# Kernel optimization log

Measured on AMD Instinct MI355X. Metric: run time of the kernel, lower is better.

Reference implementation:

```python
import jax, jax.numpy as jnp
import numpy as np

B, S, D, C = 8, 2048, 1024, 4096

def setup_inputs() -> dict:
    key = jax.random.key(0)
    k1, k2 = jax.random.split(key)
    x = jax.random.normal(k1, (B, S, D), dtype=jnp.float32)
    label_repr = jax.random.normal(k2, (C, D), dtype=jnp.float32)
    return {"x": x, "label_repr": label_repr}

def reference(x, label_repr):
    # A = softmax(x @ label_repr^T) over label axis: [B,S,C]
    scores = jnp.einsum('bsd,cd->bsc', x, label_repr)
    A = jax.nn.softmax(scores, axis=-1)
    # output = A^T @ x : [B,C,D]
    output = jnp.einsum('bsc,bsd->bcd', A, x)
    return (output, A)
```

## Files before the change

### kernel.cpp

```cpp
#include <hip/hip_runtime.h>
#include <hip/hip_bf16.h>

#define NB 8
#define NS 2048
#define ND 1024
#define NC 4096
#define NM (NB*NS)

typedef __attribute__((ext_vector_type(8))) short bf16x8;
typedef __attribute__((ext_vector_type(4))) float floatx4;
typedef unsigned short ushort_t;

__device__ __forceinline__ unsigned short f2bf(float f) {
  unsigned int u = __builtin_bit_cast(unsigned int, f);
  u += 0x7fffu + ((u >> 16) & 1u);
  return (unsigned short)(u >> 16);
}
__device__ __forceinline__ float bf2f(unsigned short h) {
  unsigned int u = ((unsigned int)h) << 16;
  return __builtin_bit_cast(float, u);
}

__device__ __forceinline__ void load_lds16(const void* g, void* s) {
  __builtin_amdgcn_global_load_lds(
      (const __attribute__((address_space(1))) char*)g,
      (__attribute__((address_space(3))) char*)s, 16, 0, 0);
}


__global__ __launch_bounds__(256)
void prep_L(const float* __restrict__ L, ushort_t* __restrict__ Lh,
            ushort_t* __restrict__ Ll) {
  const size_t i = ((size_t)blockIdx.x * 256 + threadIdx.x) * 4;
  float4 v = *(const float4*)(L + i);
  ushort4 h, lo;
  h.x = f2bf(v.x); lo.x = f2bf(v.x - bf2f(h.x));
  h.y = f2bf(v.y); lo.y = f2bf(v.y - bf2f(h.y));
  h.z = f2bf(v.z); lo.z = f2bf(v.z - bf2f(h.z));
  h.w = f2bf(v.w); lo.w = f2bf(v.w - bf2f(h.w));
  *(ushort4*)(Lh + i) = h;
  *(ushort4*)(Ll + i) = lo;
}

__global__ __launch_bounds__(256)
void prep_x(const float* __restrict__ x, ushort_t* __restrict__ xh,
            ushort_t* __restrict__ xl, ushort_t* __restrict__ xT) {
  __shared__ unsigned int tile[256 * 17];
  const int b = blockIdx.z;
  const int s0 = blockIdx.y << 5;
  const int d0 = blockIdx.x << 8;
  const int tid = threadIdx.x;
  const int sp = tid & 15, cg = tid >> 4;
  const int r0 = 2 * sp, r1 = r0 + 1;
  const float* xb = x + (size_t)b * NS * ND;
  ushort_t* xhb = xh + (size_t)b * NS * ND;
  ushort_t* xlb = xl + (size_t)b * NS * ND;
  #pragma unroll
  for (int i = 0; i < 4; ++i) {
    const int crel = cg * 4 + i * 64;
    const int col = d0 + crel;
    float4 v0 = *(const float4*)(xb + (size_t)(s0 + r0) * ND + col);
    float4 v1 = *(const float4*)(xb + (size_t)(s0 + r1) * ND + col);
    ushort4 h0, l0, h1, l1;
    h0.x = f2bf(v0.x); l0.x = f2bf(v0.x - bf2f(h0.x));
    h0.y = f2bf(v0.y); l0.y = f2bf(v0.y - bf2f(h0.y));
    h0.z = f2bf(v0.z); l0.z = f2bf(v0.z - bf2f(h0.z));
    h0.w = f2bf(v0.w); l0.w = f2bf(v0.w - bf2f(h0.w));
    h1.x = f2bf(v1.x); l1.x = f2bf(v1.x - bf2f(h1.x));
    h1.y = f2bf(v1.y); l1.y = f2bf(v1.y - bf2f(h1.y));
    h1.z = f2bf(v1.z); l1.z = f2bf(v1.z - bf2f(h1.z));
    h1.w = f2bf(v1.w); l1.w = f2bf(v1.w - bf2f(h1.w));
    *(ushort4*)(xhb + (size_t)(s0 + r0) * ND + col) = h0;
    *(ushort4*)(xlb + (size_t)(s0 + r0) * ND + col) = l0;
    *(ushort4*)(xhb + (size_t)(s0 + r1) * ND + col) = h1;
    *(ushort4*)(xlb + (size_t)(s0 + r1) * ND + col) = l1;
    tile[(crel + 0) * 17 + sp] = (unsigned)h0.x | ((unsigned)h1.x << 16);
    tile[(crel + 1) * 17 + sp] = (unsigned)h0.y | ((unsigned)h1.y << 16);
    tile[(crel + 2) * 17 + sp] = (unsigned)h0.z | ((unsigned)h1.z << 16);
    tile[(crel + 3) * 17 + sp] = (unsigned)h0.w | ((unsigned)h1.w << 16);
  }
  __syncthreads();
  unsigned tmp[16];
  #pragma unroll
  for (int k = 0; k < 16; ++k) tmp[k] = tile[tid * 17 + k];
  ushort_t* dst = xT + ((size_t)b * ND + d0 + tid) * NS + s0;
  #pragma unroll
  for (int k = 0; k < 4; ++k) *(uint4*)(dst + k * 8) = *(uint4*)&tmp[k * 4];
}

__global__ __launch_bounds__(256, 2)
void gemm1_v2(const ushort_t* __restrict__ xh, const ushort_t* __restrict__ xl,
              const ushort_t* __restrict__ Lh, const ushort_t* __restrict__ Ll,
              float* __restrict__ sc) {
  __shared__ ushort_t sAh[128 * 32];
  __shared__ ushort_t sAl[128 * 32];
  __shared__ ushort_t sBh[128 * 32];
  __shared__ ushort_t sBl[128 * 32];
  const int tid = threadIdx.x;
  const int m0 = blockIdx.y << 7;
  const int n0 = blockIdx.x << 7;
  const int w = tid >> 6, l = tid & 63;
  const int wm = (w >> 1) << 6;
  const int wn = (w & 1) << 6;
  const int lrow = l & 15, quad = l >> 4;
  const int srow = l >> 2;
  const int skol = (l & 3) << 3;

  floatx4 acc[4][4] = {};

  for (int k0 = 0; k0 < ND; k0 += 32) {
    __syncthreads();
    #pragma unroll
    for (int q = 0; q < 2; ++q) {
      const int row = w * 32 + q * 16 + srow;
      const size_t ga = (size_t)(m0 + row) * ND + k0 + skol;
      const size_t gb = (size_t)(n0 + row) * ND + k0 + skol;
      const int lo = w * 1024 + q * 512;
      load_lds16(xh + ga, &sAh[lo]);
      load_lds16(xl + ga, &sAl[lo]);
      load_lds16(Lh + gb, &sBh[lo]);
      load_lds16(Ll + gb, &sBl[lo]);
    }
    __syncthreads();
    bf16x8 ah[4], bh[4], t[4];
    #pragma unroll
    for (int i = 0; i < 4; ++i) ah[i] = *(const bf16x8*)&sAh[(wm + i*16 + lrow)*32 + quad*8];
    #pragma unroll
    for (int j = 0; j < 4; ++j) bh[j] = *(const bf16x8*)&sBh[(wn + j*16 + lrow)*32 + quad*8];
    #pragma unroll
    for (int i = 0; i < 4; ++i)
      #pragma unroll
      for (int j = 0; j < 4; ++j)
        acc[i][j] = __builtin_amdgcn_mfma_f32_16x16x32_bf16(ah[i], bh[j], acc[i][j], 0, 0, 0);
    #pragma unroll
    for (int i = 0; i < 4; ++i) t[i] = *(const bf16x8*)&sAl[(wm + i*16 + lrow)*32 + quad*8];
    #pragma unroll
    for (int i = 0; i < 4; ++i)
      #pragma unroll
      for (int j = 0; j < 4; ++j)
        acc[i][j] = __builtin_amdgcn_mfma_f32_16x16x32_bf16(t[i], bh[j], acc[i][j], 0, 0, 0);
    #pragma unroll
    for (int j = 0; j < 4; ++j) t[j] = *(const bf16x8*)&sBl[(wn + j*16 + lrow)*32 + quad*8];
    #pragma unroll
    for (int i = 0; i < 4; ++i)
      #pragma unroll
      for (int j = 0; j < 4; ++j)
        acc[i][j] = __builtin_amdgcn_mfma_f32_16x16x32_bf16(ah[i], t[j], acc[i][j], 0, 0, 0);
  }

  float* op = sc + (size_t)(m0 + wm + quad * 4) * NC + (n0 + wn + lrow);
  #pragma unroll
  for (int i = 0; i < 4; ++i)
    #pragma unroll
    for (int r = 0; r < 4; ++r)
      #pragma unroll
      for (int j = 0; j < 4; ++j)
        op[(size_t)(i * 16 + r) * NC + j * 16] = acc[i][j][r];
}

__global__ __launch_bounds__(256)
void softmax_T(float* __restrict__ A, ushort_t* __restrict__ AT) {
  __shared__ float sm[32], sli[32];
  __shared__ unsigned int tile[256 * 17];
  const int s0 = blockIdx.x << 5;
  const int b = s0 >> 11;
  const int sl0 = s0 & (NS - 1);
  const int tid = threadIdx.x;
  const int w = tid >> 6, l = tid & 63;

  float m[8], su[8];
  #pragma unroll
  for (int r = 0; r < 8; ++r) { m[r] = -3.0e38f; su[r] = 0.f; }
  for (int ch = 0; ch < 16; ++ch) {
    #pragma unroll
    for (int r = 0; r < 8; ++r) {
      float4 v = *(const float4*)(A + (size_t)(s0 + w * 8 + r) * NC + ch * 256 + (l << 2));
      float mx = fmaxf(fmaxf(v.x, v.y), fmaxf(v.z, v.w));
      float nm = fmaxf(m[r], mx);
      su[r] = su[r] * __expf(m[r] - nm) +
              __expf(v.x - nm) + __expf(v.y - nm) + __expf(v.z - nm) + __expf(v.w - nm);
      m[r] = nm;
    }
  }
  #pragma unroll
  for (int r = 0; r < 8; ++r) {
    #pragma unroll
    for (int off = 32; off; off >>= 1) {
      float om = __shfl_xor(m[r], off);
      float os = __shfl_xor(su[r], off);
      float nm = fmaxf(m[r], om);
      su[r] = su[r] * __expf(m[r] - nm) + os * __expf(om - nm);
      m[r] = nm;
    }
    if (l == 0) { sm[w * 8 + r] = m[r]; sli[w * 8 + r] = 1.0f / su[r]; }
  }
  __syncthreads();

  const int sp = tid & 15, cg = tid >> 4;
  const int r0 = 2 * sp, r1 = r0 + 1;
  const float M0 = sm[r0], I0 = sli[r0];
  const float M1 = sm[r1], I1 = sli[r1];
  float* A0 = A + (size_t)(s0 + r0) * NC;
  float* A1 = A + (size_t)(s0 + r1) * NC;
  for (int ch = 0; ch < 16; ++ch) {
    const int cb = ch << 8;
    #pragma unroll
    for (int i = 0; i < 4; ++i) {
      const int crel = cg * 4 + i * 64;
      float4 v0 = *(const float4*)(A0 + cb + crel);
      float4 v1 = *(const float4*)(A1 + cb + crel);
      float4 p0, p1;
      p0.x = __expf(v0.x - M0) * I0; p0.y = __expf(v0.y - M0) * I0;
      p0.z = __expf(v0.z - M0) * I0; p0.w = __expf(v0.w - M0) * I0;
      p1.x = __expf(v1.x - M1) * I1; p1.y = __expf(v1.y - M1) * I1;
      p1.z = __expf(v1.z - M1) * I1; p1.w = __expf(v1.w - M1) * I1;
      *(float4*)(A0 + cb + crel) = p0;
      *(float4*)(A1 + cb + crel) = p1;
      tile[(crel + 0) * 17 + sp] = (unsigned)f2bf(p0.x) | ((unsigned)f2bf(p1.x) << 16);
      tile[(crel + 1) * 17 + sp] = (unsigned)f2bf(p0.y) | ((unsigned)f2bf(p1.y) << 16);
      tile[(crel + 2) * 17 + sp] = (unsigned)f2bf(p0.z) | ((unsigned)f2bf(p1.z) << 16);
      tile[(crel + 3) * 17 + sp] = (unsigned)f2bf(p0.w) | ((unsigned)f2bf(p1.w) << 16);
    }
    __syncthreads();
    unsigned tmp[16];
    #pragma unroll
    for (int k = 0; k < 16; ++k) tmp[k] = tile[tid * 17 + k];
    ushort_t* dst = AT + ((size_t)b * NC + cb + tid) * NS + sl0;
    #pragma unroll
    for (int k = 0; k < 4; ++k) *(uint4*)(dst + k * 8) = *(uint4*)&tmp[k * 4];
    __syncthreads();
  }
}

__global__ __launch_bounds__(256, 2)
void gemm2_v2(const ushort_t* __restrict__ AT, const ushort_t* __restrict__ xT,
              float* __restrict__ out) {
  __shared__ ushort_t sA[128 * 32];
  __shared__ ushort_t sX[128 * 32];
  const int tid = threadIdx.x;
  const int b = blockIdx.z;
  const ushort_t* Ab = AT + (size_t)b * NC * NS;
  const ushort_t* xb = xT + (size_t)b * ND * NS;
  float* ob = out + (size_t)b * NC * ND;
  const int m0 = blockIdx.y << 7;
  const int n0 = blockIdx.x << 7;
  const int w = tid >> 6, l = tid & 63;
  const int wm = (w >> 1) << 6;
  const int wn = (w & 1) << 6;
  const int lrow = l & 15, quad = l >> 4;
  const int srow = l >> 2;
  const int skol = (l & 3) << 3;

  floatx4 acc[4][4] = {};

  for (int k0 = 0; k0 < NS; k0 += 32) {
    __syncthreads();
    #pragma unroll
    for (int q = 0; q < 2; ++q) {
      const int row = w * 32 + q * 16 + srow;
      const int lo = w * 1024 + q * 512;
      load_lds16(Ab + (size_t)(m0 + row) * NS + k0 + skol, &sA[lo]);
      load_lds16(xb + (size_t)(n0 + row) * NS + k0 + skol, &sX[lo]);
    }
    __syncthreads();
    bf16x8 af[4], bg[4];
    #pragma unroll
    for (int i = 0; i < 4; ++i) af[i] = *(const bf16x8*)&sA[(wm + i*16 + lrow)*32 + quad*8];
    #pragma unroll
    for (int j = 0; j < 4; ++j) bg[j] = *(const bf16x8*)&sX[(wn + j*16 + lrow)*32 + quad*8];
    #pragma unroll
    for (int i = 0; i < 4; ++i)
      #pragma unroll
      for (int j = 0; j < 4; ++j)
        acc[i][j] = __builtin_amdgcn_mfma_f32_16x16x32_bf16(af[i], bg[j], acc[i][j], 0, 0, 0);
  }

  float* op = ob + (size_t)(m0 + wm + quad * 4) * ND + (n0 + wn + lrow);
  #pragma unroll
  for (int i = 0; i < 4; ++i)
    #pragma unroll
    for (int r = 0; r < 4; ++r)
      #pragma unroll
      for (int j = 0; j < 4; ++j)
        op[(size_t)(i * 16 + r) * ND + j * 16] = acc[i][j][r];
}


__global__ __launch_bounds__(256, 2)
void gemm1_scores(const float* __restrict__ x, const float* __restrict__ L,
                  float* __restrict__ sc) {
  __shared__ unsigned short sAh[128*40];
  __shared__ unsigned short sAl[128*40];
  __shared__ unsigned short sBh[128*40];
  __shared__ unsigned short sBl[128*40];
  const int tid = threadIdx.x;
  const int m0 = blockIdx.y << 7;
  const int n0 = blockIdx.x << 7;
  const int w  = tid >> 6;
  const int l  = tid & 63;
  const int wm = (w >> 1) << 6;
  const int wn = (w & 1) << 6;
  const int lrow = l & 15;
  const int quad = l >> 4;
  floatx4 acc[4][4] = {};
  const int srow = tid >> 3;
  const int scol = (tid & 7) << 2;
  const float* xa = x + (size_t)(m0 + srow) * ND + scol;
  const float* lb = L + (size_t)(n0 + srow) * ND + scol;
  for (int k0 = 0; k0 < ND; k0 += 32) {
    float4 av[4], bv[4];
    #pragma unroll
    for (int p = 0; p < 4; ++p) {
      av[p] = *(const float4*)(xa + (size_t)(p*32) * ND + k0);
      bv[p] = *(const float4*)(lb + (size_t)(p*32) * ND + k0);
    }
    __syncthreads();
    #pragma unroll
    for (int p = 0; p < 4; ++p) {
      const int r = srow + p*32;
      ushort4 h, lo;
      h.x = f2bf(av[p].x); lo.x = f2bf(av[p].x - bf2f(h.x));
      h.y = f2bf(av[p].y); lo.y = f2bf(av[p].y - bf2f(h.y));
      h.z = f2bf(av[p].z); lo.z = f2bf(av[p].z - bf2f(h.z));
      h.w = f2bf(av[p].w); lo.w = f2bf(av[p].w - bf2f(h.w));
      *(ushort4*)&sAh[r*40 + scol] = h;
      *(ushort4*)&sAl[r*40 + scol] = lo;
      h.x = f2bf(bv[p].x); lo.x = f2bf(bv[p].x - bf2f(h.x));
      h.y = f2bf(bv[p].y); lo.y = f2bf(bv[p].y - bf2f(h.y));
      h.z = f2bf(bv[p].z); lo.z = f2bf(bv[p].z - bf2f(h.z));
      h.w = f2bf(bv[p].w); lo.w = f2bf(bv[p].w - bf2f(h.w));
      *(ushort4*)&sBh[r*40 + scol] = h;
      *(ushort4*)&sBl[r*40 + scol] = lo;
    }
    __syncthreads();
    bf16x8 ah[4], bh[4], t[4];
    #pragma unroll
    for (int i = 0; i < 4; ++i) ah[i] = *(const bf16x8*)&sAh[(wm + i*16 + lrow)*40 + quad*8];
    #pragma unroll
    for (int j = 0; j < 4; ++j) bh[j] = *(const bf16x8*)&sBh[(wn + j*16 + lrow)*40 + quad*8];
    #pragma unroll
    for (int i = 0; i < 4; ++i)
      #pragma unroll
      for (int j = 0; j < 4; ++j)
        acc[i][j] = __builtin_amdgcn_mfma_f32_16x16x32_bf16(ah[i], bh[j], acc[i][j], 0, 0, 0);
    #pragma unroll
    for (int i = 0; i < 4; ++i) t[i] = *(const bf16x8*)&sAl[(wm + i*16 + lrow)*40 + quad*8];
    #pragma unroll
    for (int i = 0; i < 4; ++i)
      #pragma unroll
      for (int j = 0; j < 4; ++j)
        acc[i][j] = __builtin_amdgcn_mfma_f32_16x16x32_bf16(t[i], bh[j], acc[i][j], 0, 0, 0);
    #pragma unroll
    for (int j = 0; j < 4; ++j) t[j] = *(const bf16x8*)&sBl[(wn + j*16 + lrow)*40 + quad*8];
    #pragma unroll
    for (int i = 0; i < 4; ++i)
      #pragma unroll
      for (int j = 0; j < 4; ++j)
        acc[i][j] = __builtin_amdgcn_mfma_f32_16x16x32_bf16(ah[i], t[j], acc[i][j], 0, 0, 0);
  }
  float* op = sc + (size_t)(m0 + wm + quad*4) * NC + (n0 + wn + lrow);
  #pragma unroll
  for (int i = 0; i < 4; ++i)
    #pragma unroll
    for (int r = 0; r < 4; ++r)
      #pragma unroll
      for (int j = 0; j < 4; ++j)
        op[(size_t)(i*16 + r) * NC + j*16] = acc[i][j][r];
}

__global__ __launch_bounds__(256)
void softmax_rows(float* __restrict__ A) {
  float* row = A + (size_t)blockIdx.x * NC;
  const int tid = threadIdx.x;
  float4 v[4];
  float mx = -3.0e38f;
  #pragma unroll
  for (int i = 0; i < 4; ++i) {
    v[i] = *(const float4*)(row + (tid << 2) + (i << 10));
    mx = fmaxf(mx, fmaxf(fmaxf(v[i].x, v[i].y), fmaxf(v[i].z, v[i].w)));
  }
  #pragma unroll
  for (int off = 32; off > 0; off >>= 1) mx = fmaxf(mx, __shfl_xor(mx, off));
  __shared__ float red[4];
  if ((tid & 63) == 0) red[tid >> 6] = mx;
  __syncthreads();
  mx = fmaxf(fmaxf(red[0], red[1]), fmaxf(red[2], red[3]));
  float s = 0.f;
  #pragma unroll
  for (int i = 0; i < 4; ++i) {
    v[i].x = __expf(v[i].x - mx); v[i].y = __expf(v[i].y - mx);
    v[i].z = __expf(v[i].z - mx); v[i].w = __expf(v[i].w - mx);
    s += (v[i].x + v[i].y) + (v[i].z + v[i].w);
  }
  #pragma unroll
  for (int off = 32; off > 0; off >>= 1) s += __shfl_xor(s, off);
  __syncthreads();
  if ((tid & 63) == 0) red[tid >> 6] = s;
  __syncthreads();
  s = (red[0] + red[1]) + (red[2] + red[3]);
  const float inv = 1.0f / s;
  #pragma unroll
  for (int i = 0; i < 4; ++i) {
    v[i].x *= inv; v[i].y *= inv; v[i].z *= inv; v[i].w *= inv;
    *(float4*)(row + (tid << 2) + (i << 10)) = v[i];
  }
}

__global__ __launch_bounds__(256, 2)
void gemm2_out(const float* __restrict__ A, const float* __restrict__ x,
               float* __restrict__ out) {
  __shared__ unsigned short sA[128*40];
  __shared__ unsigned short sX[128*40];
  const int tid = threadIdx.x;
  const float* Ab = A + (size_t)blockIdx.z * NS * NC;
  const float* xb = x + (size_t)blockIdx.z * NS * ND;
  float* ob = out + (size_t)blockIdx.z * NC * ND;
  const int m0 = blockIdx.y << 7;
  const int n0 = blockIdx.x << 7;
  const int w  = tid >> 6;
  const int l  = tid & 63;
  const int wm = (w >> 1) << 6;
  const int wn = (w & 1) << 6;
  const int lrow = l & 15;
  const int quad = l >> 4;
  floatx4 acc[4][4] = {};
  const int sp0 = tid & 15;
  const int cg0 = tid >> 4;
  for (int k0 = 0; k0 < NS; k0 += 32) {
    float4 a[2][2], xv[2][2];
    const int s = k0 + sp0*2;
    #pragma unroll
    for (int p = 0; p < 2; ++p) {
      const int c4 = (cg0 + p*16) << 2;
      a[p][0]  = *(const float4*)(Ab + (size_t)s     * NC + m0 + c4);
      a[p][1]  = *(const float4*)(Ab + (size_t)(s+1) * NC + m0 + c4);
      xv[p][0] = *(const float4*)(xb + (size_t)s     * ND + n0 + c4);
      xv[p][1] = *(const float4*)(xb + (size_t)(s+1) * ND + n0 + c4);
    }
    __syncthreads();
    #pragma unroll
    for (int p = 0; p < 2; ++p) {
      const int c4 = (cg0 + p*16) << 2;
      const float* fa0 = (const float*)&a[p][0];
      const float* fa1 = (const float*)&a[p][1];
      const float* fx0 = (const float*)&xv[p][0];
      const float* fx1 = (const float*)&xv[p][1];
      #pragma unroll
      for (int i = 0; i < 4; ++i) {
        const unsigned int pa = (unsigned int)f2bf(fa0[i]) | ((unsigned int)f2bf(fa1[i]) << 16);
        const unsigned int px = (unsigned int)f2bf(fx0[i]) | ((unsigned int)f2bf(fx1[i]) << 16);
        *(unsigned int*)&sA[(c4 + i)*40 + sp0*2] = pa;
        *(unsigned int*)&sX[(c4 + i)*40 + sp0*2] = px;
      }
    }
    __syncthreads();
    bf16x8 af[4], bg[4];
    #pragma unroll
    for (int i = 0; i < 4; ++i) af[i] = *(const bf16x8*)&sA[(wm + i*16 + lrow)*40 + quad*8];
    #pragma unroll
    for (int j = 0; j < 4; ++j) bg[j] = *(const bf16x8*)&sX[(wn + j*16 + lrow)*40 + quad*8];
    #pragma unroll
    for (int i = 0; i < 4; ++i)
      #pragma unroll
      for (int j = 0; j < 4; ++j)
        acc[i][j] = __builtin_amdgcn_mfma_f32_16x16x32_bf16(af[i], bg[j], acc[i][j], 0, 0, 0);
  }
  float* op = ob + (size_t)(m0 + wm + quad*4) * ND + (n0 + wn + lrow);
  #pragma unroll
  for (int i = 0; i < 4; ++i)
    #pragma unroll
    for (int r = 0; r < 4; ++r)
      #pragma unroll
      for (int j = 0; j < 4; ++j)
        op[(size_t)(i*16 + r) * ND + j*16] = acc[i][j][r];
}


extern "C" void kernel_launch(void* const* d_in, const int* in_sizes, int n_in,
                              void* d_out, int out_size, void* d_ws, size_t ws_size,
                              hipStream_t stream) {
  const float* x = (const float*)d_in[0];
  const float* L = (const float*)d_in[1];
  float* out = (float*)d_out;
  float* A   = out + (size_t)NB * NC * ND;

  const size_t EL_X  = (size_t)NB * NS * ND;
  const size_t EL_L  = (size_t)NC * ND;
  const size_t EL_AT = (size_t)NB * NC * NS;
  const size_t need  = (3 * EL_X + 2 * EL_L + EL_AT) * sizeof(ushort_t);

  if (ws_size >= need) {
    ushort_t* xh = (ushort_t*)d_ws;
    ushort_t* xl = xh + EL_X;
    ushort_t* xT = xl + EL_X;
    ushort_t* Lh = xT + EL_X;
    ushort_t* Ll = Lh + EL_L;
    ushort_t* AT = Ll + EL_L;
    prep_L<<<dim3((NC * ND) / 1024), 256, 0, stream>>>(L, Lh, Ll);
    prep_x<<<dim3(ND / 256, NS / 32, NB), 256, 0, stream>>>(x, xh, xl, xT);
    gemm1_v2<<<dim3(NC / 128, NM / 128), 256, 0, stream>>>(xh, xl, Lh, Ll, A);
    softmax_T<<<dim3(NM / 32), 256, 0, stream>>>(A, AT);
    gemm2_v2<<<dim3(ND / 128, NC / 128, NB), 256, 0, stream>>>(AT, xT, out);
  } else {
    gemm1_scores<<<dim3(NC / 128, NM / 128), 256, 0, stream>>>(x, L, A);
    softmax_rows<<<dim3(NM), 256, 0, stream>>>(A);
    gemm2_out<<<dim3(ND / 128, NC / 128, NB), 256, 0, stream>>>(A, x, out);
  }
}
```

Measured before the change: 1.166 ms.

## Fuse softmax row stats into GEMM1 epilogue and swizzle LDS tiles

GEMM1 now computes a per-tile row max and sum-of-exp in its epilogue and writes them to scratch space in the output buffer. The softmax kernel merges these partials, so it no longer does a full read pass over the scores. Both GEMMs also switch to a combined, XOR-swizzled LDS layout to avoid bank conflicts, and GEMM2 now uses a K step of 64. The costs are that the partials share the output buffer before GEMM2 overwrites it, and GEMM1 gains shuffles and an extra sync in its epilogue.

```diff
diff --git a/kernel.cpp b/kernel.cpp
--- a/kernel.cpp
+++ b/kernel.cpp
@@ -89,13 +89,12 @@
 }
 
 __global__ __launch_bounds__(256, 2)
-void gemm1_v2(const ushort_t* __restrict__ xh, const ushort_t* __restrict__ xl,
+void gemm1_v3(const ushort_t* __restrict__ xh, const ushort_t* __restrict__ xl,
               const ushort_t* __restrict__ Lh, const ushort_t* __restrict__ Ll,
-              float* __restrict__ sc) {
-  __shared__ ushort_t sAh[128 * 32];
-  __shared__ ushort_t sAl[128 * 32];
-  __shared__ ushort_t sBh[128 * 32];
-  __shared__ ushort_t sBl[128 * 32];
+              float* __restrict__ sc, float* __restrict__ pmax,
+              float* __restrict__ psum) {
+  __shared__ ushort_t sA[128 * 64];
+  __shared__ ushort_t sB[128 * 64];
   const int tid = threadIdx.x;
   const int m0 = blockIdx.y << 7;
   const int n0 = blockIdx.x << 7;
@@ -103,44 +102,45 @@
   const int wm = (w >> 1) << 6;
   const int wn = (w & 1) << 6;
   const int lrow = l & 15, quad = l >> 4;
-  const int srow = l >> 2;
-  const int skol = (l & 3) << 3;
+
+  const int rsub = l >> 3;
+  const int kg   = (l & 7) ^ rsub;
+  const int koff = (kg & 3) << 3;
+  const ushort_t* pax = (kg & 4) ? xl : xh;
+  const ushort_t* pbx = (kg & 4) ? Ll : Lh;
+
+  const int sw = (quad ^ (lrow & 7)) << 3;
 
   floatx4 acc[4][4] = {};
 
   for (int k0 = 0; k0 < ND; k0 += 32) {
     __syncthreads();
     #pragma unroll
-    for (int q = 0; q < 2; ++q) {
-      const int row = w * 32 + q * 16 + srow;
-      const size_t ga = (size_t)(m0 + row) * ND + k0 + skol;
-      const size_t gb = (size_t)(n0 + row) * ND + k0 + skol;
-      const int lo = w * 1024 + q * 512;
-      load_lds16(xh + ga, &sAh[lo]);
-      load_lds16(xl + ga, &sAl[lo]);
-      load_lds16(Lh + gb, &sBh[lo]);
-      load_lds16(Ll + gb, &sBl[lo]);
+    for (int q = 0; q < 4; ++q) {
+      const int row = ((w * 4 + q) << 3) + rsub;
+      load_lds16(pax + (size_t)(m0 + row) * ND + k0 + koff, &sA[(w * 4 + q) * 512]);
+      load_lds16(pbx + (size_t)(n0 + row) * ND + k0 + koff, &sB[(w * 4 + q) * 512]);
     }
     __syncthreads();
     bf16x8 ah[4], bh[4], t[4];
     #pragma unroll
-    for (int i = 0; i < 4; ++i) ah[i] = *(const bf16x8*)&sAh[(wm + i*16 + lrow)*32 + quad*8];
-    #pragma unroll
-    for (int j = 0; j < 4; ++j) bh[j] = *(const bf16x8*)&sBh[(wn + j*16 + lrow)*32 + quad*8];
+    for (int i = 0; i < 4; ++i) ah[i] = *(const bf16x8*)&sA[(wm + i*16 + lrow)*64 + sw];
+    #pragma unroll
+    for (int j = 0; j < 4; ++j) bh[j] = *(const bf16x8*)&sB[(wn + j*16 + lrow)*64 + sw];
     #pragma unroll
     for (int i = 0; i < 4; ++i)
       #pragma unroll
       for (int j = 0; j < 4; ++j)
         acc[i][j] = __builtin_amdgcn_mfma_f32_16x16x32_bf16(ah[i], bh[j], acc[i][j], 0, 0, 0);
     #pragma unroll
-    for (int i = 0; i < 4; ++i) t[i] = *(const bf16x8*)&sAl[(wm + i*16 + lrow)*32 + quad*8];
+    for (int i = 0; i < 4; ++i) t[i] = *(const bf16x8*)&sA[(wm + i*16 + lrow)*64 + (sw ^ 32)];
     #pragma unroll
     for (int i = 0; i < 4; ++i)
       #pragma unroll
       for (int j = 0; j < 4; ++j)
         acc[i][j] = __builtin_amdgcn_mfma_f32_16x16x32_bf16(t[i], bh[j], acc[i][j], 0, 0, 0);
     #pragma unroll
-    for (int j = 0; j < 4; ++j) t[j] = *(const bf16x8*)&sBl[(wn + j*16 + lrow)*32 + quad*8];
+    for (int j = 0; j < 4; ++j) t[j] = *(const bf16x8*)&sB[(wn + j*16 + lrow)*64 + (sw ^ 32)];
     #pragma unroll
     for (int i = 0; i < 4; ++i)
       #pragma unroll
@@ -156,43 +156,59 @@
       #pragma unroll
       for (int j = 0; j < 4; ++j)
         op[(size_t)(i * 16 + r) * NC + j * 16] = acc[i][j][r];
+
+  __syncthreads();
+  float* lmax = (float*)sA;
+  float* lsum = (float*)sB;
+  #pragma unroll
+  for (int i = 0; i < 4; ++i)
+    #pragma unroll
+    for (int r = 0; r < 4; ++r) {
+      float mx = fmaxf(fmaxf(acc[i][0][r], acc[i][1][r]),
+                       fmaxf(acc[i][2][r], acc[i][3][r]));
+      #pragma unroll
+      for (int off = 1; off < 16; off <<= 1) mx = fmaxf(mx, __shfl_xor(mx, off));
+      float se = __expf(acc[i][0][r] - mx) + __expf(acc[i][1][r] - mx) +
+                 __expf(acc[i][2][r] - mx) + __expf(acc[i][3][r] - mx);
+      #pragma unroll
+      for (int off = 1; off < 16; off <<= 1) se += __shfl_xor(se, off);
+      if (lrow == 0) {
+        const int rl = wm + i * 16 + quad * 4 + r;
+        lmax[rl * 2 + (wn >> 6)] = mx;
+        lsum[rl * 2 + (wn >> 6)] = se;
+      }
+    }
+  __syncthreads();
+  if (tid < 128) {
+    const float ma = lmax[tid * 2], mb = lmax[tid * 2 + 1];
+    const float M = fmaxf(ma, mb);
+    const float Z = lsum[tid * 2] * __expf(ma - M) + lsum[tid * 2 + 1] * __expf(mb - M);
+    pmax[(size_t)blockIdx.x * NM + m0 + tid] = M;
+    psum[(size_t)blockIdx.x * NM + m0 + tid] = Z;
+  }
 }
 
 __global__ __launch_bounds__(256)
-void softmax_T(float* __restrict__ A, ushort_t* __restrict__ AT) {
+void softmax_T(float* __restrict__ A, const float* __restrict__ pmax,
+               const float* __restrict__ psum, ushort_t* __restrict__ AT) {
   __shared__ float sm[32], sli[32];
   __shared__ unsigned int tile[256 * 17];
   const int s0 = blockIdx.x << 5;
   const int b = s0 >> 11;
   const int sl0 = s0 & (NS - 1);
   const int tid = threadIdx.x;
-  const int w = tid >> 6, l = tid & 63;
-
-  float m[8], su[8];
-  #pragma unroll
-  for (int r = 0; r < 8; ++r) { m[r] = -3.0e38f; su[r] = 0.f; }
-  for (int ch = 0; ch < 16; ++ch) {
-    #pragma unroll
-    for (int r = 0; r < 8; ++r) {
-      float4 v = *(const float4*)(A + (size_t)(s0 + w * 8 + r) * NC + ch * 256 + (l << 2));
-      float mx = fmaxf(fmaxf(v.x, v.y), fmaxf(v.z, v.w));
-      float nm = fmaxf(m[r], mx);
-      su[r] = su[r] * __expf(m[r] - nm) +
-              __expf(v.x - nm) + __expf(v.y - nm) + __expf(v.z - nm) + __expf(v.w - nm);
-      m[r] = nm;
-    }
-  }
-  #pragma unroll
-  for (int r = 0; r < 8; ++r) {
-    #pragma unroll
-    for (int off = 32; off; off >>= 1) {
-      float om = __shfl_xor(m[r], off);
-      float os = __shfl_xor(su[r], off);
-      float nm = fmaxf(m[r], om);
-      su[r] = su[r] * __expf(m[r] - nm) + os * __expf(om - nm);
-      m[r] = nm;
-    }
-    if (l == 0) { sm[w * 8 + r] = m[r]; sli[w * 8 + r] = 1.0f / su[r]; }
+
+  if (tid < 32) {
+    const int row = s0 + tid;
+    float M = -3.0e38f, Z = 0.f;
+    for (int n = 0; n < NC / 128; ++n) {
+      const float pm = pmax[(size_t)n * NM + row];
+      const float ps = psum[(size_t)n * NM + row];
+      const float nm = fmaxf(M, pm);
+      Z = Z * __expf(M - nm) + ps * __expf(pm - nm);
+      M = nm;
+    }
+    sm[tid] = M; sli[tid] = 1.0f / Z;
   }
   __syncthreads();
 
@@ -233,10 +249,10 @@
 }
 
 __global__ __launch_bounds__(256, 2)
-void gemm2_v2(const ushort_t* __restrict__ AT, const ushort_t* __restrict__ xT,
+void gemm2_v3(const ushort_t* __restrict__ AT, const ushort_t* __restrict__ xT,
               float* __restrict__ out) {
-  __shared__ ushort_t sA[128 * 32];
-  __shared__ ushort_t sX[128 * 32];
+  __shared__ ushort_t sA[128 * 64];
+  __shared__ ushort_t sX[128 * 64];
   const int tid = threadIdx.x;
   const int b = blockIdx.z;
   const ushort_t* Ab = AT + (size_t)b * NC * NS;
@@ -248,31 +264,35 @@
   const int wm = (w >> 1) << 6;
   const int wn = (w & 1) << 6;
   const int lrow = l & 15, quad = l >> 4;
-  const int srow = l >> 2;
-  const int skol = (l & 3) << 3;
+
+  const int rsub = l >> 3;
+  const int kg = (l & 7) ^ rsub;
 
   floatx4 acc[4][4] = {};
 
-  for (int k0 = 0; k0 < NS; k0 += 32) {
-    __syncthreads();
-    #pragma unroll
-    for (int q = 0; q < 2; ++q) {
-      const int row = w * 32 + q * 16 + srow;
-      const int lo = w * 1024 + q * 512;
-      load_lds16(Ab + (size_t)(m0 + row) * NS + k0 + skol, &sA[lo]);
-      load_lds16(xb + (size_t)(n0 + row) * NS + k0 + skol, &sX[lo]);
-    }
-    __syncthreads();
-    bf16x8 af[4], bg[4];
-    #pragma unroll
-    for (int i = 0; i < 4; ++i) af[i] = *(const bf16x8*)&sA[(wm + i*16 + lrow)*32 + quad*8];
-    #pragma unroll
-    for (int j = 0; j < 4; ++j) bg[j] = *(const bf16x8*)&sX[(wn + j*16 + lrow)*32 + quad*8];
-    #pragma unroll
-    for (int i = 0; i < 4; ++i)
-      #pragma unroll
-      for (int j = 0; j < 4; ++j)
-        acc[i][j] = __builtin_amdgcn_mfma_f32_16x16x32_bf16(af[i], bg[j], acc[i][j], 0, 0, 0);
+  for (int k0 = 0; k0 < NS; k0 += 64) {
+    __syncthreads();
+    #pragma unroll
+    for (int q = 0; q < 4; ++q) {
+      const int row = ((w * 4 + q) << 3) + rsub;
+      load_lds16(Ab + (size_t)(m0 + row) * NS + k0 + kg * 8, &sA[(w * 4 + q) * 512]);
+      load_lds16(xb + (size_t)(n0 + row) * NS + k0 + kg * 8, &sX[(w * 4 + q) * 512]);
+    }
+    __syncthreads();
+    #pragma unroll
+    for (int h = 0; h < 2; ++h) {
+      const int sw = ((h * 4 + quad) ^ (lrow & 7)) << 3;
+      bf16x8 af[4], bg[4];
+      #pragma unroll
+      for (int i = 0; i < 4; ++i) af[i] = *(const bf16x8*)&sA[(wm + i*16 + lrow)*64 + sw];
+      #pragma unroll
+      for (int j = 0; j < 4; ++j) bg[j] = *(const bf16x8*)&sX[(wn + j*16 + lrow)*64 + sw];
+      #pragma unroll
+      for (int i = 0; i < 4; ++i)
+        #pragma unroll
+        for (int j = 0; j < 4; ++j)
+          acc[i][j] = __builtin_amdgcn_mfma_f32_16x16x32_bf16(af[i], bg[j], acc[i][j], 0, 0, 0);
+    }
   }
 
   float* op = ob + (size_t)(m0 + wm + quad * 4) * ND + (n0 + wn + lrow);
@@ -496,11 +516,13 @@
     ushort_t* Lh = xT + EL_X;
     ushort_t* Ll = Lh + EL_L;
     ushort_t* AT = Ll + EL_L;
+    float* pmax = out;
+    float* psum = out + (size_t)(NC / 128) * NM;
     prep_L<<<dim3((NC * ND) / 1024), 256, 0, stream>>>(L, Lh, Ll);
     prep_x<<<dim3(ND / 256, NS / 32, NB), 256, 0, stream>>>(x, xh, xl, xT);
-    gemm1_v2<<<dim3(NC / 128, NM / 128), 256, 0, stream>>>(xh, xl, Lh, Ll, A);
-    softmax_T<<<dim3(NM / 32), 256, 0, stream>>>(A, AT);
-    gemm2_v2<<<dim3(ND / 128, NC / 128, NB), 256, 0, stream>>>(AT, xT, out);
+    gemm1_v3<<<dim3(NC / 128, NM / 128), 256, 0, stream>>>(xh, xl, Lh, Ll, A, pmax, psum);
+    softmax_T<<<dim3(NM / 32), 256, 0, stream>>>(A, pmax, psum, AT);
+    gemm2_v3<<<dim3(ND / 128, NC / 128, NB), 256, 0, stream>>>(AT, xT, out);
   } else {
     gemm1_scores<<<dim3(NC / 128, NM / 128), 256, 0, stream>>>(x, L, A);
     softmax_rows<<<dim3(NM), 256, 0, stream>>>(A);
```

Result: faster. 1.125 ms (-3.5%).
